# Kernel optimization log

Hardware: AMD Instinct MI355X
Metric: run time of the kernel (lower is better)

## Reference

```python
import jax, jax.numpy as jnp
import numpy as np


def setup_inputs() -> dict:
    key = jax.random.key(0)
    k1, k2 = jax.random.split(key)
    B, D, T = 16, 256, 2048
    L, K = 8, 1024
    x = jax.random.normal(k1, (B, D, T), dtype=jnp.float32)
    codebooks = jax.random.normal(k2, (L, K, D), dtype=jnp.float32)
    return {"x": x, "codebooks": codebooks}


def reference(x, codebooks):
    """Residual vector quantization (SoundStream-style).

    x:         (B, D, T) latent features
    codebooks: (L, K, D) one codebook per residual layer

    Returns:
        output:  (B, D, T) sum of selected embeddings across layers
        indices: (B, L, T) selected codebook indices per layer
    """
    r0 = jnp.transpose(x, (0, 2, 1))  # (B, T, D)

    def step(carry, W):
        residual, acc = carry
        # squared euclidean distance: ||r||^2 - 2 r.W^T + ||w||^2  -> (B, T, K)
        dots = jnp.einsum("btd,kd->btk", residual, W)
        dist = (
            jnp.sum(residual * residual, axis=-1, keepdims=True)
            - 2.0 * dots
            + jnp.sum(W * W, axis=-1)
        )
        idx = jnp.argmin(dist, axis=-1)          # (B, T)
        q = W[idx]                               # (B, T, D) gather
        return (residual - q, acc + q), idx

    (_, quantized), indices = jax.lax.scan(
        step, (r0, jnp.zeros_like(r0)), codebooks
    )
    output = jnp.transpose(quantized, (0, 2, 1))        # (B, D, T)
    indices = jnp.transpose(indices, (1, 0, 2))          # (B, L, T)
    return output, indices
```

## Files before the change

kernel.cpp:

```cpp
#include <hip/hip_runtime.h>

#define D_ 256
#define T_ 2048
#define K_ 1024
#define L_ 8
#define B_ 16
#define THETA 0.5f
#define ECT 40
#define NTILE 256

typedef _Float16 f16x8 __attribute__((ext_vector_type(8)));
typedef float    f32x4 __attribute__((ext_vector_type(4)));

typedef const __attribute__((address_space(1))) unsigned int* gas1_t;
typedef __attribute__((address_space(3))) unsigned int*       las3_t;

__device__ __forceinline__ void gls16(const void* g, void* l) {
    __builtin_amdgcn_global_load_lds((gas1_t)g, (las3_t)l, 16, 0, 0);
}
__device__ __forceinline__ void gls4(const void* g, void* l) {
    __builtin_amdgcn_global_load_lds((gas1_t)g, (las3_t)l, 4, 0, 0);
}

__device__ __forceinline__ unsigned long long packkey(float sc, unsigned cand) {
    const unsigned fb = __float_as_uint(sc);
    const unsigned ob = fb ^ ((unsigned)((int)fb >> 31) | 0x80000000u);
    return (((unsigned long long)ob) << 32) | cand;
}
__device__ __forceinline__ float unpackf(unsigned long long key) {
    const unsigned ob = (unsigned)(key >> 32);
    const unsigned fb = (ob & 0x80000000u) ? (ob ^ 0x80000000u) : ~ob;
    return __uint_as_float(fb);
}
__device__ __forceinline__ unsigned short f2h_bits(float s) {
    union { _Float16 f; unsigned short u; } cv; cv.f = (_Float16)s; return cv.u;
}
__device__ __forceinline__ float h_bits2f(unsigned short u) {
    union { _Float16 f; unsigned short u; } cv; cv.u = u; return (float)cv.f;
}

__global__ __launch_bounds__(256, 4)
void rvq_ww_kernel(const float* __restrict__ cb, float* __restrict__ ww) {
    const int row  = blockIdx.x * 4 + (threadIdx.x >> 6);
    const int lane = threadIdx.x & 63;
    const float4 v = *reinterpret_cast<const float4*>(cb + (size_t)row * D_ + (lane << 2));
    float s = v.x * v.x + v.y * v.y + v.z * v.z + v.w * v.w;
    #pragma unroll
    for (int off = 1; off < 64; off <<= 1) s += __shfl_xor(s, off, 64);
    if (lane == 0) ww[row] = s;
}

__global__ __launch_bounds__(256)
void rvq_cvtp_kernel(const float* __restrict__ cb, _Float16* __restrict__ cbp) {
    const int e    = blockIdx.x * 256 + threadIdx.x;
    const int lane = e & 63, sub = (e >> 6) & 15, ch = (e >> 10) & 31, l = e >> 15;
    const int n = sub & 1, kk = sub >> 1, g = lane >> 4, c4 = lane & 15;
    const float* src = cb + (size_t)(l * 1024 + ch * 32 + n * 16 + c4) * D_ + kk * 32 + g * 8;
    const float4 a = *reinterpret_cast<const float4*>(src);
    const float4 b = *reinterpret_cast<const float4*>(src + 4);
    f16x8 v;
    v[0] = (_Float16)a.x; v[1] = (_Float16)a.y; v[2] = (_Float16)a.z; v[3] = (_Float16)a.w;
    v[4] = (_Float16)b.x; v[5] = (_Float16)b.y; v[6] = (_Float16)b.z; v[7] = (_Float16)b.w;
    *reinterpret_cast<f16x8*>(cbp + (size_t)e * 8) = v;
}

__global__ __launch_bounds__(256, 2)
void rvq_main_kernel(const float* __restrict__ x, const float* __restrict__ cbf,
                     const _Float16* __restrict__ cb16p, const float* __restrict__ ww,
                     float* __restrict__ out) {
    __shared__ __align__(16) _Float16 bstage[3][8192];
    __shared__ float    wwlds[3][64];
    __shared__ unsigned elist[4][16][ECT];
    __shared__ int      ecnt[4][16];

    const int tid  = threadIdx.x;
    const int lane = tid & 63;
    const int wv   = tid >> 6;
    const int c4   = lane & 15;
    const int g    = lane >> 4;
    const int tg   = blockIdx.x * 64 + wv * 16 + c4;
    const int b    = tg >> 11;
    const int tl   = tg & (T_ - 1);
    const size_t xbase = ((size_t)b << 19) + tl;

    auto stage_tile = [&](int gt) {
        const int bufi = gt % 3;
        const _Float16* s = cb16p + ((size_t)gt * 1024 + wv * 256 + lane) * 8;
        char* d = (char*)bstage[bufi] + wv * 4096;
        #pragma unroll
        for (int i = 0; i < 4; ++i)
            gls16(s + i * 512, d + i * 1024);
        gls4(ww + gt * 32 + lane, &wwlds[bufi][0]);
    };

    stage_tile(0);
    stage_tile(1);

    float r_[64];
    #pragma unroll
    for (int kk = 0; kk < 8; ++kk)
        #pragma unroll
        for (int e = 0; e < 8; ++e)
            r_[kk * 8 + e] = x[xbase + (size_t)(kk * 32 + g * 8 + e) * T_];

    #pragma unroll 1
    for (int l = 0; l < L_; ++l) {
        const float* __restrict__ cblf = cbf + (size_t)l * K_ * D_;
        const float* __restrict__ wwl  = ww + l * K_;

        if (lane < 16) ecnt[wv][lane] = 0;

        float rrv;
        {
            float Tk[8];
            #pragma unroll
            for (int kk = 0; kk < 8; ++kk) {
                float4 v;
                v.x = r_[kk * 8 + 0]; v.y = r_[kk * 8 + 1];
                v.z = r_[kk * 8 + 2]; v.w = r_[kk * 8 + 3];
                float s = v.x * v.x + v.y * v.y + v.z * v.z + v.w * v.w;
                float4 u;
                u.x = r_[kk * 8 + 4]; u.y = r_[kk * 8 + 5];
                u.z = r_[kk * 8 + 6]; u.w = r_[kk * 8 + 7];
                float s2 = u.x * u.x + u.y * u.y + u.z * u.z + u.w * u.w;
                const float p  = s + s2;
                const float po = __shfl_xor(p, 16, 64);
                const float q  = p + po;
                const float qo = __shfl_xor(q, 32, 64);
                Tk[kk] = q + qo;
            }
            const float u01 = Tk[0] + Tk[1], u23 = Tk[2] + Tk[3];
            const float u45 = Tk[4] + Tk[5], u67 = Tk[6] + Tk[7];
            rrv = (u01 + u23) + (u45 + u67);
        }

        f16x8 fr[8];
        #pragma unroll
        for (int kk = 0; kk < 8; ++kk)
            #pragma unroll
            for (int e = 0; e < 8; ++e)
                fr[kk][e] = (_Float16)r_[kk * 8 + e];

        unsigned long long bkl[4];
        float bth[4];
        #pragma unroll
        for (int j = 0; j < 4; ++j) {
            bkl[j] = packkey(__builtin_inff(), 0u);
            bth[j] = __builtin_inff();
        }

        asm volatile("s_waitcnt vmcnt(0)" ::: "memory");
        __builtin_amdgcn_s_barrier();

        #pragma unroll 1
        for (int c = 0; c < 32; ++c) {
            const int gt   = l * 32 + c;
            const int bufi = gt % 3;
            const bool pf  = (gt + 2 < NTILE);
            if (pf) stage_tile(gt + 2);

            const _Float16* bufp = bstage[bufi];
            const int base = c * 32;
            f32x4 acc0 = (f32x4){0.f, 0.f, 0.f, 0.f};
            f32x4 acc1 = (f32x4){0.f, 0.f, 0.f, 0.f};

            #pragma unroll
            for (int kk = 0; kk < 8; ++kk) {
                const f16x8 b0 = *reinterpret_cast<const f16x8*>(
                    bufp + ((kk * 2 + 0) * 64 + lane) * 8);
                const f16x8 b1 = *reinterpret_cast<const f16x8*>(
                    bufp + ((kk * 2 + 1) * 64 + lane) * 8);
                acc0 = __builtin_amdgcn_mfma_f32_16x16x32_f16(fr[kk], b0, acc0, 0, 0, 0);
                acc1 = __builtin_amdgcn_mfma_f32_16x16x32_f16(fr[kk], b1, acc1, 0, 0, 0);
            }

            const float ww0 = wwlds[bufi][c4];
            const float ww1 = wwlds[bufi][16 + c4];

            #pragma unroll
            for (int n2 = 0; n2 < 2; ++n2) {
                const f32x4 av = n2 ? acc1 : acc0;
                const unsigned cand = (unsigned)(base + n2 * 16 + c4);
                const float wwv = n2 ? ww1 : ww0;
                #pragma unroll
                for (int j = 0; j < 4; ++j) {
                    const float sc = fmaf(-2.0f, av[j], wwv);
                    const unsigned long long key = packkey(sc, cand);
                    const int tj = g * 4 + j;
                    if (key < bkl[j]) {
                        const float old = unpackf(bkl[j]);
                        if (old <= sc + THETA) {
                            const int p = atomicAdd(&ecnt[wv][tj], 1);
                            if (p < ECT)
                                elist[wv][tj][p] =
                                    (((unsigned)(bkl[j] & 0xffffull)) << 16) | f2h_bits(old);
                        }
                        bkl[j] = key;
                        bth[j] = sc + THETA;
                    } else if (sc <= bth[j]) {
                        const int p = atomicAdd(&ecnt[wv][tj], 1);
                        if (p < ECT)
                            elist[wv][tj][p] = (cand << 16) | f2h_bits(sc);
                    }
                }
            }

            if (pf) { asm volatile("s_waitcnt vmcnt(6)" ::: "memory"); }
            else    { asm volatile("s_waitcnt vmcnt(0)" ::: "memory"); }
            __builtin_amdgcn_s_barrier();
        }

        unsigned long long gk[4];
        #pragma unroll
        for (int j = 0; j < 4; ++j) {
            unsigned long long k0 = bkl[j];
            #pragma unroll
            for (int off = 1; off < 16; off <<= 1) {
                const unsigned long long k2 = __shfl_xor(k0, off, 64);
                if (k2 < k0) k0 = k2;
            }
            gk[j] = k0;
            if (bkl[j] != k0) {
                const float ls = unpackf(bkl[j]);
                if (ls <= unpackf(k0) + THETA) {
                    const int tj = g * 4 + j;
                    const int p = atomicAdd(&ecnt[wv][tj], 1);
                    if (p < ECT)
                        elist[wv][tj][p] =
                            (((unsigned)(bkl[j] & 0xffffull)) << 16) | f2h_bits(ls);
                }
            }
        }

        unsigned bc0 = (unsigned)(gk[0] & 0xffffffffull);
        unsigned bc1 = (unsigned)(gk[1] & 0xffffffffull);
        unsigned bc2 = (unsigned)(gk[2] & 0xffffffffull);
        unsigned bc3 = (unsigned)(gk[3] & 0xffffffffull);
        float gm0 = unpackf(gk[0]), gm1 = unpackf(gk[1]);
        float gm2 = unpackf(gk[2]), gm3 = unpackf(gk[3]);
        const int srcl = (c4 >> 2) << 4;
        const unsigned w0 = __shfl(bc0, srcl, 64);
        const unsigned w1 = __shfl(bc1, srcl, 64);
        const unsigned w2 = __shfl(bc2, srcl, 64);
        const unsigned w3 = __shfl(bc3, srcl, 64);
        const float s0 = __shfl(gm0, srcl, 64);
        const float s1 = __shfl(gm1, srcl, 64);
        const float s2 = __shfl(gm2, srcl, 64);
        const float s3 = __shfl(gm3, srcl, 64);
        const unsigned wa = (c4 & 1) ? w1 : w0;
        const unsigned wb = (c4 & 1) ? w3 : w2;
        const unsigned wincand = (c4 & 2) ? wb : wa;
        const float sa = (c4 & 1) ? s1 : s0;
        const float sb = (c4 & 1) ? s3 : s2;
        const float gminmy = (c4 & 2) ? sb : sa;

        unsigned long long bestk;
        {
            const float* wp = cblf + (size_t)wincand * D_;
            float4 wA = *reinterpret_cast<const float4*>(wp + g * 8);
            float4 wB = *reinterpret_cast<const float4*>(wp + g * 8 + 4);
            float4 nA = *reinterpret_cast<const float4*>(wp + 32 + g * 8);
            float4 nB = *reinterpret_cast<const float4*>(wp + 32 + g * 8 + 4);
            float a0 = 0.0f;
            #pragma unroll
            for (int s = 0; s < 32; ++s) {
                const int kk = s >> 2;
                if ((s & 3) == g) {
                    a0 = fmaf(wA.x, r_[kk * 8 + 0], a0);
                    a0 = fmaf(wA.y, r_[kk * 8 + 1], a0);
                    a0 = fmaf(wA.z, r_[kk * 8 + 2], a0);
                    a0 = fmaf(wA.w, r_[kk * 8 + 3], a0);
                    a0 = fmaf(wB.x, r_[kk * 8 + 4], a0);
                    a0 = fmaf(wB.y, r_[kk * 8 + 5], a0);
                    a0 = fmaf(wB.z, r_[kk * 8 + 6], a0);
                    a0 = fmaf(wB.w, r_[kk * 8 + 7], a0);
                    wA = nA; wB = nB;
                    if (kk + 2 < 8) {
                        nA = *reinterpret_cast<const float4*>(wp + (kk + 2) * 32 + g * 8);
                        nB = *reinterpret_cast<const float4*>(wp + (kk + 2) * 32 + g * 8 + 4);
                    }
                }
                a0 = __shfl(a0, (lane + 48) & 63, 64);
            }
            a0 = __shfl(a0, c4, 64);
            const float scw = __fadd_rn(__fsub_rn(rrv, __fmul_rn(2.0f, a0)), wwl[wincand]);
            bestk = packkey(scw, wincand);
        }

        {
            const int myn = min(ecnt[wv][c4], ECT);
            const float gth = gminmy + THETA + 0.5f;
            #pragma unroll 1
            for (int i = 0; i < myn; ++i) {
                const unsigned e  = elist[wv][c4][i];
                const unsigned ec = e >> 16;
                const float hsc = h_bits2f((unsigned short)(e & 0xffffu));
                if (ec == wincand || hsc > gth) continue;
                const float* ep = cblf + (size_t)ec * D_;
                float4 wA = *reinterpret_cast<const float4*>(ep + g * 8);
                float4 wB = *reinterpret_cast<const float4*>(ep + g * 8 + 4);
                float4 nA = *reinterpret_cast<const float4*>(ep + 32 + g * 8);
                float4 nB = *reinterpret_cast<const float4*>(ep + 32 + g * 8 + 4);
                float q = 0.0f;
                #pragma unroll
                for (int s = 0; s < 32; ++s) {
                    const int kk = s >> 2;
                    if ((s & 3) == g) {
                        q = fmaf(wA.x, r_[kk * 8 + 0], q);
                        q = fmaf(wA.y, r_[kk * 8 + 1], q);
                        q = fmaf(wA.z, r_[kk * 8 + 2], q);
                        q = fmaf(wA.w, r_[kk * 8 + 3], q);
                        q = fmaf(wB.x, r_[kk * 8 + 4], q);
                        q = fmaf(wB.y, r_[kk * 8 + 5], q);
                        q = fmaf(wB.z, r_[kk * 8 + 6], q);
                        q = fmaf(wB.w, r_[kk * 8 + 7], q);
                        wA = nA; wB = nB;
                        if (kk + 2 < 8) {
                            nA = *reinterpret_cast<const float4*>(ep + (kk + 2) * 32 + g * 8);
                            nB = *reinterpret_cast<const float4*>(ep + (kk + 2) * 32 + g * 8 + 4);
                        }
                    }
                    q = __shfl(q, (lane + 48) & 63, 64);
                }
                q = __shfl(q, c4, 64);
                const float sce = __fadd_rn(__fsub_rn(rrv, __fmul_rn(2.0f, q)), wwl[ec]);
                const unsigned long long k2 = packkey(sce, ec);
                if (k2 < bestk) bestk = k2;
            }
        }

        const unsigned fc = (unsigned)(bestk & 0xffffffffull);
        if (g == 0)
            out[(size_t)B_ * D_ * T_ + ((size_t)b * L_ + l) * T_ + tl] = (float)fc;

        {
            const float* up = cblf + (size_t)fc * D_;
            #pragma unroll
            for (int kk = 0; kk < 8; ++kk) {
                const float4 ua = *reinterpret_cast<const float4*>(up + kk * 32 + g * 8);
                const float4 ub = *reinterpret_cast<const float4*>(up + kk * 32 + g * 8 + 4);
                r_[kk * 8 + 0] = __fsub_rn(r_[kk * 8 + 0], ua.x);
                r_[kk * 8 + 1] = __fsub_rn(r_[kk * 8 + 1], ua.y);
                r_[kk * 8 + 2] = __fsub_rn(r_[kk * 8 + 2], ua.z);
                r_[kk * 8 + 3] = __fsub_rn(r_[kk * 8 + 3], ua.w);
                r_[kk * 8 + 4] = __fsub_rn(r_[kk * 8 + 4], ub.x);
                r_[kk * 8 + 5] = __fsub_rn(r_[kk * 8 + 5], ub.y);
                r_[kk * 8 + 6] = __fsub_rn(r_[kk * 8 + 6], ub.z);
                r_[kk * 8 + 7] = __fsub_rn(r_[kk * 8 + 7], ub.w);
            }
        }
    }

    #pragma unroll
    for (int kk = 0; kk < 8; ++kk)
        #pragma unroll
        for (int e = 0; e < 8; ++e) {
            const size_t gi = xbase + (size_t)(kk * 32 + g * 8 + e) * T_;
            out[gi] = __fsub_rn(x[gi], r_[kk * 8 + e]);
        }
}

extern "C" void kernel_launch(void* const* d_in, const int* in_sizes, int n_in,
                              void* d_out, int out_size, void* d_ws, size_t ws_size,
                              hipStream_t stream) {
    const float* x  = (const float*)d_in[0];
    const float* cb = (const float*)d_in[1];
    float* out = (float*)d_out;
    float*    ww    = (float*)d_ws;
    _Float16* cb16p = (_Float16*)((char*)d_ws + 32768);

    hipLaunchKernelGGL(rvq_ww_kernel,   dim3((L_ * K_) / 4), dim3(256), 0, stream, cb, ww);
    hipLaunchKernelGGL(rvq_cvtp_kernel, dim3(1024), dim3(256), 0, stream, cb, cb16p);
    hipLaunchKernelGGL(rvq_main_kernel, dim3((B_ * T_) / 64), dim3(256), 0, stream,
                       x, cb, cb16p, ww, out);
}
```

Measured before the change: 530.9 us.

## Widen codebook tiles to 128 codes with 512-thread blocks and double buffering

Each pipeline step now stages a 128-code codebook tile instead of a 32-code one. The block grows to 8 waves covering 128 timesteps, and each wave issues 8 MFMAs per k-slice into 8 accumulators. The fp16 packing kernel is relaid out to match the new tile shape. Triple buffering with fine-grained vmcnt waits is replaced by a double buffer synchronised with __syncthreads, so there are four times fewer barriers per layer. In exchange, shared memory per block rises to roughly 150KB, which limits each CU to one block, and the extra accumulators raise register pressure with a risk of spills.

```diff
diff --git a/kernel.cpp b/kernel.cpp
--- a/kernel.cpp
+++ b/kernel.cpp
@@ -7,7 +7,7 @@
 #define B_ 16
 #define THETA 0.5f
 #define ECT 40
-#define NTILE 256
+#define NTILE 64
 
 typedef _Float16 f16x8 __attribute__((ext_vector_type(8)));
 typedef float    f32x4 __attribute__((ext_vector_type(4)));
@@ -53,9 +53,11 @@
 __global__ __launch_bounds__(256)
 void rvq_cvtp_kernel(const float* __restrict__ cb, _Float16* __restrict__ cbp) {
     const int e    = blockIdx.x * 256 + threadIdx.x;
-    const int lane = e & 63, sub = (e >> 6) & 15, ch = (e >> 10) & 31, l = e >> 15;
-    const int n = sub & 1, kk = sub >> 1, g = lane >> 4, c4 = lane & 15;
-    const float* src = cb + (size_t)(l * 1024 + ch * 32 + n * 16 + c4) * D_ + kk * 32 + g * 8;
+    const int gt   = e >> 12, q = e & 4095;
+    const int lane = q & 63, nk = q >> 6;
+    const int n = nk & 7, kk = nk >> 3, c4 = lane & 15, g = lane >> 4;
+    const int l = gt >> 3, ch = gt & 7;
+    const float* src = cb + (size_t)(l * 1024 + ch * 128 + n * 16 + c4) * D_ + kk * 32 + g * 8;
     const float4 a = *reinterpret_cast<const float4*>(src);
     const float4 b = *reinterpret_cast<const float4*>(src + 4);
     f16x8 v;
@@ -64,37 +66,36 @@
     *reinterpret_cast<f16x8*>(cbp + (size_t)e * 8) = v;
 }
 
-__global__ __launch_bounds__(256, 2)
+__global__ __launch_bounds__(512, 2)
 void rvq_main_kernel(const float* __restrict__ x, const float* __restrict__ cbf,
                      const _Float16* __restrict__ cb16p, const float* __restrict__ ww,
                      float* __restrict__ out) {
-    __shared__ __align__(16) _Float16 bstage[3][8192];
-    __shared__ float    wwlds[3][64];
-    __shared__ unsigned elist[4][16][ECT];
-    __shared__ int      ecnt[4][16];
+    __shared__ __align__(16) _Float16 bstage[2][32768];
+    __shared__ float    wwlds[2][128];
+    __shared__ unsigned elist[8][16][ECT];
+    __shared__ int      ecnt[8][16];
 
     const int tid  = threadIdx.x;
     const int lane = tid & 63;
     const int wv   = tid >> 6;
     const int c4   = lane & 15;
     const int g    = lane >> 4;
-    const int tg   = blockIdx.x * 64 + wv * 16 + c4;
+    const int tg   = blockIdx.x * 128 + wv * 16 + c4;
     const int b    = tg >> 11;
     const int tl   = tg & (T_ - 1);
     const size_t xbase = ((size_t)b << 19) + tl;
 
     auto stage_tile = [&](int gt) {
-        const int bufi = gt % 3;
-        const _Float16* s = cb16p + ((size_t)gt * 1024 + wv * 256 + lane) * 8;
-        char* d = (char*)bstage[bufi] + wv * 4096;
-        #pragma unroll
-        for (int i = 0; i < 4; ++i)
+        const _Float16* s = cb16p + ((size_t)gt * 4096 + wv * 512 + lane) * 8;
+        char* d = (char*)bstage[gt & 1] + wv * 8192;
+        #pragma unroll
+        for (int i = 0; i < 8; ++i)
             gls16(s + i * 512, d + i * 1024);
-        gls4(ww + gt * 32 + lane, &wwlds[bufi][0]);
+        if (wv < 2)
+            gls4(ww + gt * 128 + wv * 64 + lane, &wwlds[gt & 1][wv * 64]);
     };
 
     stage_tile(0);
-    stage_tile(1);
 
     float r_[64];
     #pragma unroll
@@ -102,6 +103,8 @@
         #pragma unroll
         for (int e = 0; e < 8; ++e)
             r_[kk * 8 + e] = x[xbase + (size_t)(kk * 32 + g * 8 + e) * T_];
+
+    __syncthreads();
 
     #pragma unroll 1
     for (int l = 0; l < L_; ++l) {
@@ -149,42 +152,36 @@
             bth[j] = __builtin_inff();
         }
 
-        asm volatile("s_waitcnt vmcnt(0)" ::: "memory");
-        __builtin_amdgcn_s_barrier();
-
         #pragma unroll 1
-        for (int c = 0; c < 32; ++c) {
-            const int gt   = l * 32 + c;
-            const int bufi = gt % 3;
-            const bool pf  = (gt + 2 < NTILE);
-            if (pf) stage_tile(gt + 2);
-
-            const _Float16* bufp = bstage[bufi];
-            const int base = c * 32;
-            f32x4 acc0 = (f32x4){0.f, 0.f, 0.f, 0.f};
-            f32x4 acc1 = (f32x4){0.f, 0.f, 0.f, 0.f};
+        for (int c = 0; c < 8; ++c) {
+            const int gt = l * 8 + c;
+            if (gt + 1 < NTILE) stage_tile(gt + 1);
+
+            const _Float16* bufp = bstage[gt & 1];
+            const float*    wwp  = wwlds[gt & 1];
+            const int base = c * 128;
+
+            f32x4 acc[8];
+            #pragma unroll
+            for (int n = 0; n < 8; ++n) acc[n] = (f32x4){0.f, 0.f, 0.f, 0.f};
 
             #pragma unroll
             for (int kk = 0; kk < 8; ++kk) {
-                const f16x8 b0 = *reinterpret_cast<const f16x8*>(
-                    bufp + ((kk * 2 + 0) * 64 + lane) * 8);
-                const f16x8 b1 = *reinterpret_cast<const f16x8*>(
-                    bufp + ((kk * 2 + 1) * 64 + lane) * 8);
-                acc0 = __builtin_amdgcn_mfma_f32_16x16x32_f16(fr[kk], b0, acc0, 0, 0, 0);
-                acc1 = __builtin_amdgcn_mfma_f32_16x16x32_f16(fr[kk], b1, acc1, 0, 0, 0);
-            }
-
-            const float ww0 = wwlds[bufi][c4];
-            const float ww1 = wwlds[bufi][16 + c4];
-
-            #pragma unroll
-            for (int n2 = 0; n2 < 2; ++n2) {
-                const f32x4 av = n2 ? acc1 : acc0;
-                const unsigned cand = (unsigned)(base + n2 * 16 + c4);
-                const float wwv = n2 ? ww1 : ww0;
+                #pragma unroll
+                for (int n = 0; n < 8; ++n) {
+                    const f16x8 bf = *reinterpret_cast<const f16x8*>(
+                        bufp + ((kk * 8 + n) * 64 + lane) * 8);
+                    acc[n] = __builtin_amdgcn_mfma_f32_16x16x32_f16(fr[kk], bf, acc[n], 0, 0, 0);
+                }
+            }
+
+            #pragma unroll
+            for (int n = 0; n < 8; ++n) {
+                const unsigned cand = (unsigned)(base + n * 16 + c4);
+                const float wwv = wwp[n * 16 + c4];
                 #pragma unroll
                 for (int j = 0; j < 4; ++j) {
-                    const float sc = fmaf(-2.0f, av[j], wwv);
+                    const float sc = fmaf(-2.0f, acc[n][j], wwv);
                     const unsigned long long key = packkey(sc, cand);
                     const int tj = g * 4 + j;
                     if (key < bkl[j]) {
@@ -205,9 +202,7 @@
                 }
             }
 
-            if (pf) { asm volatile("s_waitcnt vmcnt(6)" ::: "memory"); }
-            else    { asm volatile("s_waitcnt vmcnt(0)" ::: "memory"); }
-            __builtin_amdgcn_s_barrier();
+            __syncthreads();
         }
 
         unsigned long long gk[4];
@@ -371,6 +366,6 @@
 
     hipLaunchKernelGGL(rvq_ww_kernel,   dim3((L_ * K_) / 4), dim3(256), 0, stream, cb, ww);
     hipLaunchKernelGGL(rvq_cvtp_kernel, dim3(1024), dim3(256), 0, stream, cb, cb16p);
-    hipLaunchKernelGGL(rvq_main_kernel, dim3((B_ * T_) / 64), dim3(256), 0, stream,
+    hipLaunchKernelGGL(rvq_main_kernel, dim3((B_ * T_) / 128), dim3(512), 0, stream,
                        x, cb, cb16p, ww, out);
 }
```

After: 528.9 us. Within noise of the previous version (-0.4%).

## Split codebook search across two wave groups per block with LDS argmin merge

Applied to the files above, without the earlier changes.

Doubles the block to 512 threads. Two halves of waves each scan half of the codebook (16 tiles instead of 32) for the same 64 time steps, and their best keys and exact-rescoring results are merged with LDS atomicMin. The full per-layer norm table is loaded into LDS once per layer instead of per tile, and the staging pipeline drops from triple to double buffering with __syncthreads. This aims to halve the serial scan per wave and raise occupancy, at the cost of duplicated residual state and rescoring work in both halves, extra block-wide barriers, and a smaller candidate list.

```diff
diff --git a/kernel.cpp b/kernel.cpp
--- a/kernel.cpp
+++ b/kernel.cpp
@@ -6,8 +6,7 @@
 #define L_ 8
 #define B_ 16
 #define THETA 0.5f
-#define ECT 40
-#define NTILE 256
+#define ECT 20
 
 typedef _Float16 f16x8 __attribute__((ext_vector_type(8)));
 typedef float    f32x4 __attribute__((ext_vector_type(4)));
@@ -64,37 +63,39 @@
     *reinterpret_cast<f16x8*>(cbp + (size_t)e * 8) = v;
 }
 
-__global__ __launch_bounds__(256, 2)
+__global__ __launch_bounds__(512, 4)
 void rvq_main_kernel(const float* __restrict__ x, const float* __restrict__ cbf,
                      const _Float16* __restrict__ cb16p, const float* __restrict__ ww,
                      float* __restrict__ out) {
-    __shared__ __align__(16) _Float16 bstage[3][8192];
-    __shared__ float    wwlds[3][64];
-    __shared__ unsigned elist[4][16][ECT];
-    __shared__ int      ecnt[4][16];
+    __shared__ __align__(16) _Float16 bstage[2][2][8192];
+    __shared__ float               wwall[1024];
+    __shared__ unsigned long long  fin64[64];
+    __shared__ unsigned long long  ex64[64];
+    __shared__ unsigned            elist[8][16][ECT];
+    __shared__ int                 ecnt[8][16];
 
     const int tid  = threadIdx.x;
     const int lane = tid & 63;
     const int wv   = tid >> 6;
+    const int half = wv >> 2;
+    const int grp  = wv & 3;
     const int c4   = lane & 15;
     const int g    = lane >> 4;
-    const int tg   = blockIdx.x * 64 + wv * 16 + c4;
+    const int tg   = blockIdx.x * 64 + grp * 16 + c4;
     const int b    = tg >> 11;
     const int tl   = tg & (T_ - 1);
     const size_t xbase = ((size_t)b << 19) + tl;
 
-    auto stage_tile = [&](int gt) {
-        const int bufi = gt % 3;
-        const _Float16* s = cb16p + ((size_t)gt * 1024 + wv * 256 + lane) * 8;
-        char* d = (char*)bstage[bufi] + wv * 4096;
+    auto stage_tile = [&](int l, int c) {
+        const int gt = l * 32 + half * 16 + c;
+        const _Float16* s = cb16p + ((size_t)gt * 1024 + grp * 256 + lane) * 8;
+        char* d = (char*)&bstage[half][c & 1][0] + grp * 4096;
         #pragma unroll
         for (int i = 0; i < 4; ++i)
             gls16(s + i * 512, d + i * 1024);
-        gls4(ww + gt * 32 + lane, &wwlds[bufi][0]);
     };
 
-    stage_tile(0);
-    stage_tile(1);
+    stage_tile(0, 0);
 
     float r_[64];
     #pragma unroll
@@ -106,9 +107,12 @@
     #pragma unroll 1
     for (int l = 0; l < L_; ++l) {
         const float* __restrict__ cblf = cbf + (size_t)l * K_ * D_;
-        const float* __restrict__ wwl  = ww + l * K_;
-
+
+        if (tid < 64) { fin64[tid] = ~0ull; ex64[tid] = ~0ull; }
         if (lane < 16) ecnt[wv][lane] = 0;
+        #pragma unroll
+        for (int i = 0; i < 2; ++i)
+            gls4(ww + l * 1024 + wv * 128 + i * 64 + lane, &wwall[wv * 128 + i * 64]);
 
         float rrv;
         {
@@ -149,18 +153,14 @@
             bth[j] = __builtin_inff();
         }
 
-        asm volatile("s_waitcnt vmcnt(0)" ::: "memory");
-        __builtin_amdgcn_s_barrier();
+        __syncthreads();
 
         #pragma unroll 1
-        for (int c = 0; c < 32; ++c) {
-            const int gt   = l * 32 + c;
-            const int bufi = gt % 3;
-            const bool pf  = (gt + 2 < NTILE);
-            if (pf) stage_tile(gt + 2);
-
-            const _Float16* bufp = bstage[bufi];
-            const int base = c * 32;
+        for (int c = 0; c < 16; ++c) {
+            const int s = l * 16 + c;
+            if (s + 1 < 128) stage_tile((s + 1) >> 4, (s + 1) & 15);
+
+            const _Float16* bufp = &bstage[half][c & 1][0];
             f32x4 acc0 = (f32x4){0.f, 0.f, 0.f, 0.f};
             f32x4 acc1 = (f32x4){0.f, 0.f, 0.f, 0.f};
 
@@ -174,14 +174,12 @@
                 acc1 = __builtin_amdgcn_mfma_f32_16x16x32_f16(fr[kk], b1, acc1, 0, 0, 0);
             }
 
-            const float ww0 = wwlds[bufi][c4];
-            const float ww1 = wwlds[bufi][16 + c4];
-
+            const int cbase = half * 512 + c * 32;
             #pragma unroll
             for (int n2 = 0; n2 < 2; ++n2) {
                 const f32x4 av = n2 ? acc1 : acc0;
-                const unsigned cand = (unsigned)(base + n2 * 16 + c4);
-                const float wwv = n2 ? ww1 : ww0;
+                const unsigned cand = (unsigned)(cbase + n2 * 16 + c4);
+                const float wwv = wwall[cand];
                 #pragma unroll
                 for (int j = 0; j < 4; ++j) {
                     const float sc = fmaf(-2.0f, av[j], wwv);
@@ -205,12 +203,10 @@
                 }
             }
 
-            if (pf) { asm volatile("s_waitcnt vmcnt(6)" ::: "memory"); }
-            else    { asm volatile("s_waitcnt vmcnt(0)" ::: "memory"); }
-            __builtin_amdgcn_s_barrier();
-        }
-
-        unsigned long long gk[4];
+            __syncthreads();
+        }
+
+        unsigned long long wk[4];
         #pragma unroll
         for (int j = 0; j < 4; ++j) {
             unsigned long long k0 = bkl[j];
@@ -219,7 +215,7 @@
                 const unsigned long long k2 = __shfl_xor(k0, off, 64);
                 if (k2 < k0) k0 = k2;
             }
-            gk[j] = k0;
+            wk[j] = k0;
             if (bkl[j] != k0) {
                 const float ls = unpackf(bkl[j]);
                 if (ls <= unpackf(k0) + THETA) {
@@ -230,29 +226,27 @@
                             (((unsigned)(bkl[j] & 0xffffull)) << 16) | f2h_bits(ls);
                 }
             }
-        }
-
-        unsigned bc0 = (unsigned)(gk[0] & 0xffffffffull);
-        unsigned bc1 = (unsigned)(gk[1] & 0xffffffffull);
-        unsigned bc2 = (unsigned)(gk[2] & 0xffffffffull);
-        unsigned bc3 = (unsigned)(gk[3] & 0xffffffffull);
-        float gm0 = unpackf(gk[0]), gm1 = unpackf(gk[1]);
-        float gm2 = unpackf(gk[2]), gm3 = unpackf(gk[3]);
-        const int srcl = (c4 >> 2) << 4;
-        const unsigned w0 = __shfl(bc0, srcl, 64);
-        const unsigned w1 = __shfl(bc1, srcl, 64);
-        const unsigned w2 = __shfl(bc2, srcl, 64);
-        const unsigned w3 = __shfl(bc3, srcl, 64);
-        const float s0 = __shfl(gm0, srcl, 64);
-        const float s1 = __shfl(gm1, srcl, 64);
-        const float s2 = __shfl(gm2, srcl, 64);
-        const float s3 = __shfl(gm3, srcl, 64);
-        const unsigned wa = (c4 & 1) ? w1 : w0;
-        const unsigned wb = (c4 & 1) ? w3 : w2;
-        const unsigned wincand = (c4 & 2) ? wb : wa;
-        const float sa = (c4 & 1) ? s1 : s0;
-        const float sb = (c4 & 1) ? s3 : s2;
-        const float gminmy = (c4 & 2) ? sb : sa;
+            if (c4 == 0) atomicMin(&fin64[grp * 16 + g * 4 + j], k0);
+        }
+        __syncthreads();
+
+        if (c4 == 0) {
+            #pragma unroll
+            for (int j = 0; j < 4; ++j) {
+                const unsigned long long fk = fin64[grp * 16 + g * 4 + j];
+                if (wk[j] != fk && unpackf(wk[j]) <= unpackf(fk) + THETA) {
+                    const int tj = g * 4 + j;
+                    const int p = atomicAdd(&ecnt[wv][tj], 1);
+                    if (p < ECT)
+                        elist[wv][tj][p] =
+                            (((unsigned)(wk[j] & 0xffffull)) << 16) | f2h_bits(unpackf(wk[j]));
+                }
+            }
+        }
+
+        const unsigned long long fkt = fin64[grp * 16 + c4];
+        const unsigned wincand = (unsigned)(fkt & 0xffffffffull);
+        const float    gminmy  = unpackf(fkt);
 
         unsigned long long bestk;
         {
@@ -283,7 +277,7 @@
                 a0 = __shfl(a0, (lane + 48) & 63, 64);
             }
             a0 = __shfl(a0, c4, 64);
-            const float scw = __fadd_rn(__fsub_rn(rrv, __fmul_rn(2.0f, a0)), wwl[wincand]);
+            const float scw = __fadd_rn(__fsub_rn(rrv, __fmul_rn(2.0f, a0)), wwall[wincand]);
             bestk = packkey(scw, wincand);
         }
 
@@ -323,14 +317,17 @@
                     q = __shfl(q, (lane + 48) & 63, 64);
                 }
                 q = __shfl(q, c4, 64);
-                const float sce = __fadd_rn(__fsub_rn(rrv, __fmul_rn(2.0f, q)), wwl[ec]);
+                const float sce = __fadd_rn(__fsub_rn(rrv, __fmul_rn(2.0f, q)), wwall[ec]);
                 const unsigned long long k2 = packkey(sce, ec);
                 if (k2 < bestk) bestk = k2;
             }
         }
 
-        const unsigned fc = (unsigned)(bestk & 0xffffffffull);
-        if (g == 0)
+        if (g == 0) atomicMin(&ex64[grp * 16 + c4], bestk);
+        __syncthreads();
+
+        const unsigned fc = (unsigned)(ex64[grp * 16 + c4] & 0xffffffffull);
+        if (g == 0 && half == 0)
             out[(size_t)B_ * D_ * T_ + ((size_t)b * L_ + l) * T_ + tl] = (float)fc;
 
         {
@@ -349,15 +346,18 @@
                 r_[kk * 8 + 7] = __fsub_rn(r_[kk * 8 + 7], ub.w);
             }
         }
+        __syncthreads();
     }
 
-    #pragma unroll
-    for (int kk = 0; kk < 8; ++kk)
-        #pragma unroll
-        for (int e = 0; e < 8; ++e) {
-            const size_t gi = xbase + (size_t)(kk * 32 + g * 8 + e) * T_;
-            out[gi] = __fsub_rn(x[gi], r_[kk * 8 + e]);
-        }
+    if (half == 0) {
+        #pragma unroll
+        for (int kk = 0; kk < 8; ++kk)
+            #pragma unroll
+            for (int e = 0; e < 8; ++e) {
+                const size_t gi = xbase + (size_t)(kk * 32 + g * 8 + e) * T_;
+                out[gi] = __fsub_rn(x[gi], r_[kk * 8 + e]);
+            }
+    }
 }
 
 extern "C" void kernel_launch(void* const* d_in, const int* in_sizes, int n_in,
@@ -371,6 +371,6 @@
 
     hipLaunchKernelGGL(rvq_ww_kernel,   dim3((L_ * K_) / 4), dim3(256), 0, stream, cb, ww);
     hipLaunchKernelGGL(rvq_cvtp_kernel, dim3(1024), dim3(256), 0, stream, cb, cb16p);
-    hipLaunchKernelGGL(rvq_main_kernel, dim3((B_ * T_) / 64), dim3(256), 0, stream,
+    hipLaunchKernelGGL(rvq_main_kernel, dim3((B_ * T_) / 64), dim3(512), 0, stream,
                        x, cb, cb16p, ww, out);
 }
```

Measured after the change: 617.9 us. 1.16x slower.
